# Kernel optimization log

Hardware: AMD Instinct MI355X
Metric: run time of the kernel (lower is better)

## Reference

```python
import jax, jax.numpy as jnp
import numpy as np

N, E, H, C = 50000, 1_600_000, 4, 32
DIN, DE = 128, 32
NEG_SLOPE = 0.2  # PyG GATConv leaky_relu negative_slope default


def setup_inputs() -> dict:
    key = jax.random.key(0)
    ks = jax.random.split(key, 12)
    s = 0.1  # weight scale
    return {
        "x": jax.random.normal(ks[0], (N, DIN), jnp.float32),
        "edge_index": jax.random.randint(ks[1], (2, E), 0, N, jnp.int32),
        "edge_attr": jax.random.normal(ks[2], (E, DE), jnp.float32),
        "W": jax.random.normal(ks[3], (DIN, H * C), jnp.float32) * s,
        "att_src": jax.random.normal(ks[4], (H, C), jnp.float32) * s,
        "att_dst": jax.random.normal(ks[5], (H, C), jnp.float32) * s,
        "lin_edge_W": jax.random.normal(ks[6], (DE, H * C), jnp.float32) * s,
        "att_edge": jax.random.normal(ks[7], (H, C), jnp.float32) * s,
        "bias": jax.random.normal(ks[8], (H * C,), jnp.float32) * s,
        "proj_W": jax.random.normal(ks[9], (H * C, C), jnp.float32) * s,
        "proj_b": jax.random.normal(ks[10], (C,), jnp.float32) * s,
    }


def reference(x, edge_index, edge_attr, W, att_src, att_dst, lin_edge_W,
              att_edge, bias, proj_W, proj_b):
    n = x.shape[0]
    h, c = att_src.shape
    src, dst = edge_index[0], edge_index[1]

    # add self loops; loop edge_attr = mean of incoming edge_attr (PyG fill_value='mean')
    deg = jax.ops.segment_sum(jnp.ones(src.shape, x.dtype), dst, num_segments=n)
    ea_mean = jax.ops.segment_sum(edge_attr, dst, num_segments=n) / jnp.maximum(deg, 1.0)[:, None]
    loop = jnp.arange(n, dtype=src.dtype)
    src = jnp.concatenate([src, loop])
    dst = jnp.concatenate([dst, loop])
    ea = jnp.concatenate([edge_attr, ea_mean], axis=0)

    xl = (x @ W).reshape(n, h, c)                       # [N,H,C]
    a_src = jnp.einsum('nhc,hc->nh', xl, att_src)       # [N,H]
    a_dst = jnp.einsum('nhc,hc->nh', xl, att_dst)
    e = (ea @ lin_edge_W).reshape(-1, h, c)             # [E',H,C]
    a_e = jnp.einsum('ehc,hc->eh', e, att_edge)

    alpha = jax.nn.leaky_relu(a_src[src] + a_dst[dst] + a_e, NEG_SLOPE)  # [E',H]
    amax = jax.lax.stop_gradient(jax.ops.segment_max(alpha, dst, num_segments=n))
    alpha = jnp.exp(alpha - amax[dst])
    denom = jax.ops.segment_sum(alpha, dst, num_segments=n)
    alpha = alpha / (denom[dst] + 1e-16)                # segment softmax over incoming edges

    out = jax.ops.segment_sum(xl[src] * alpha[..., None], dst, num_segments=n)  # [N,H,C]
    out = out.reshape(n, h * c) + bias                  # concat heads + bias
    return out @ proj_W + proj_b                        # concat projection
```

## Files before the change

### kernel.cpp

```cpp
#include <hip/hip_runtime.h>

#define NEG_SLOPE 0.2f

typedef float f32x4 __attribute__((ext_vector_type(4)));
typedef short bf16x8 __attribute__((ext_vector_type(8)));

__device__ __forceinline__ float lrelu(float x) { return x > 0.0f ? x : NEG_SLOPE * x; }

__device__ __forceinline__ float bcast(float v, int srcLane) {
  return __int_as_float(__builtin_amdgcn_readlane(__float_as_int(v), srcLane));
}

__device__ __forceinline__ unsigned pack_bf16(float a, float b) {
  unsigned ua = __float_as_uint(a), ub = __float_as_uint(b);
  ua += 0x7fffu + ((ua >> 16) & 1u);
  ub += 0x7fffu + ((ub >> 16) & 1u);
  return (ua >> 16) | (ub & 0xffff0000u);
}
__device__ __forceinline__ unsigned short bf16of(float a) {
  unsigned ua = __float_as_uint(a);
  ua += 0x7fffu + ((ua >> 16) & 1u);
  return (unsigned short)(ua >> 16);
}
__device__ __forceinline__ float bf16lo(unsigned z) { return __uint_as_float(z << 16); }
__device__ __forceinline__ float bf16hi(unsigned z) { return __uint_as_float(z & 0xffff0000u); }

__global__ void k0_setup(const float* __restrict__ W, const float* __restrict__ proj_W,
                         const float* __restrict__ att_src, const float* __restrict__ att_dst,
                         const float* __restrict__ lin_edge_W, const float* __restrict__ att_edge,
                         const float* __restrict__ bias, const float* __restrict__ proj_b,
                         unsigned short* __restrict__ Wzb, float* __restrict__ Ws,
                         float* __restrict__ Wd, float* __restrict__ M, float* __restrict__ cproj) {
  int t = blockIdx.x * blockDim.x + threadIdx.x;
  if (t < 16384) {
    int d = t >> 7, o = t & 127;
    int h = o >> 5, jj = o & 31;
    float s = 0.f;
    #pragma unroll
    for (int c = 0; c < 32; ++c)
      s += W[d * 128 + h * 32 + c] * proj_W[(h * 32 + c) * 32 + jj];
    Wzb[((d >> 3) * 128 + o) * 8 + (d & 7)] = bf16of(s);
  } else if (t < 16384 + 512) {
    int idx = t - 16384; int d = idx >> 2, h = idx & 3;
    float s = 0.f;
    #pragma unroll
    for (int c = 0; c < 32; ++c) s += W[d * 128 + h * 32 + c] * att_src[h * 32 + c];
    Ws[d * 4 + h] = s;
  } else if (t < 16384 + 1024) {
    int idx = t - 16384 - 512; int d = idx >> 2, h = idx & 3;
    float s = 0.f;
    #pragma unroll
    for (int c = 0; c < 32; ++c) s += W[d * 128 + h * 32 + c] * att_dst[h * 32 + c];
    Wd[d * 4 + h] = s;
  } else if (t < 16384 + 1024 + 128) {
    int idx = t - 16384 - 1024; int d = idx >> 2, h = idx & 3;
    float s = 0.f;
    #pragma unroll
    for (int c = 0; c < 32; ++c) s += lin_edge_W[d * 128 + h * 32 + c] * att_edge[h * 32 + c];
    M[d * 4 + h] = s;
  } else if (t < 16384 + 1024 + 128 + 32) {
    int jj = t - 16384 - 1024 - 128;
    float s = proj_b[jj];
    #pragma unroll
    for (int k = 0; k < 128; ++k) s += bias[k] * proj_W[k * 32 + jj];
    cproj[jj] = s;
  }
}

__global__ __launch_bounds__(256) void k3a_att(
    const float* __restrict__ x, const float* __restrict__ Ws, const float* __restrict__ Wd,
    int n, float* __restrict__ a_src, float* __restrict__ a_dst) {
  int tid = threadIdx.x;
  int lane = tid & 63, wid = tid >> 6;
  float ws0[4], ws1[4], wd0[4], wd1[4];
  #pragma unroll
  for (int h = 0; h < 4; ++h) {
    ws0[h] = Ws[lane * 4 + h];  ws1[h] = Ws[(64 + lane) * 4 + h];
    wd0[h] = Wd[lane * 4 + h];  wd1[h] = Wd[(64 + lane) * 4 + h];
  }
  int gw = blockIdx.x * 4 + wid;
  int nw = gridDim.x * 4;
  for (int base = gw * 4; base < n; base += nw * 4) {
    float xa[4], xb[4];
    #pragma unroll
    for (int u = 0; u < 4; ++u) {
      int node = base + u;
      xa[u] = (node < n) ? x[(size_t)node * 128 + lane] : 0.0f;
      xb[u] = (node < n) ? x[(size_t)node * 128 + 64 + lane] : 0.0f;
    }
    #pragma unroll
    for (int u = 0; u < 4; ++u) {
      int node = base + u;
      if (node >= n) break;
      float ps[4], pd[4];
      #pragma unroll
      for (int h = 0; h < 4; ++h) {
        ps[h] = xa[u] * ws0[h] + xb[u] * ws1[h];
        pd[h] = xa[u] * wd0[h] + xb[u] * wd1[h];
      }
      #pragma unroll
      for (int m = 1; m < 64; m <<= 1) {
        #pragma unroll
        for (int h = 0; h < 4; ++h) {
          ps[h] += __shfl_xor(ps[h], m);
          pd[h] += __shfl_xor(pd[h], m);
        }
      }
      if (lane == 0) {
        *(float4*)&a_src[node * 4] = make_float4(ps[0], ps[1], ps[2], ps[3]);
        *(float4*)&a_dst[node * 4] = make_float4(pd[0], pd[1], pd[2], pd[3]);
      }
    }
  }
}

__global__ __launch_bounds__(256) void k3b_gemm(
    const float* __restrict__ x, const unsigned short* __restrict__ Wzb,
    int n, unsigned* __restrict__ Zp) {
  __shared__ __align__(16) unsigned short WzL[16384];
  int tid = threadIdx.x;
  #pragma unroll
  for (int i = 0; i < 8; ++i)
    *(uint4*)&WzL[(i * 256 + tid) * 8] = *(const uint4*)&Wzb[(i * 256 + tid) * 8];
  __syncthreads();
  int lane = tid & 63, wid = tid >> 6;
  int rgrp = lane >> 4, rl = lane & 15;
  int r0 = blockIdx.x * 64 + wid * 16;
  if (r0 >= n) return;
  int row = r0 + rl; if (row >= n) row = n - 1;
  const float* xr = x + (size_t)row * 128 + rgrp * 8;
  bf16x8 a[4];
  #pragma unroll
  for (int q = 0; q < 4; ++q) {
    float4 v0 = *(const float4*)(xr + q * 32);
    float4 v1 = *(const float4*)(xr + q * 32 + 4);
    union { unsigned u[4]; bf16x8 v; } fa;
    fa.u[0] = pack_bf16(v0.x, v0.y); fa.u[1] = pack_bf16(v0.z, v0.w);
    fa.u[2] = pack_bf16(v1.x, v1.y); fa.u[3] = pack_bf16(v1.z, v1.w);
    a[q] = fa.v;
  }
  f32x4 acc[8];
  #pragma unroll
  for (int t = 0; t < 8; ++t) acc[t] = (f32x4){0.f, 0.f, 0.f, 0.f};
  #pragma unroll
  for (int q = 0; q < 4; ++q) {
    #pragma unroll
    for (int t = 0; t < 8; ++t) {
      bf16x8 b = *(const bf16x8*)&WzL[((q * 4 + rgrp) * 128 + t * 16 + rl) * 8];
      acc[t] = __builtin_amdgcn_mfma_f32_16x16x32_bf16(a[q], b, acc[t], 0, 0, 0);
    }
  }
  #pragma unroll
  for (int t = 0; t < 4; ++t) {
    #pragma unroll
    for (int r = 0; r < 4; ++r) {
      int rr = r0 + rgrp * 4 + r;
      if (rr < n)
        Zp[(size_t)rr * 64 + t * 16 + rl] = pack_bf16(acc[t][r], acc[t + 4][r]);
    }
  }
}

__global__ __launch_bounds__(256) void k1_edge(
    const int* __restrict__ ei, int E, const float4* __restrict__ ea4,
    const float* __restrict__ Mg,
    const float* __restrict__ a_src, const float* __restrict__ a_dst,
    uint4* __restrict__ we, int* __restrict__ deg, int* __restrict__ rank) {
  int lane = threadIdx.x & 63, wid = threadIdx.x >> 6;
  int j = lane & 7;
  const float4* Mf4 = (const float4*)Mg;
  float4 m0 = Mf4[4 * j + 0], m1 = Mf4[4 * j + 1];
  float4 m2 = Mf4[4 * j + 2], m3 = Mf4[4 * j + 3];
  int perm = 8 * (lane & 7) + (lane >> 3);
  int gw = blockIdx.x * 4 + wid, nw = gridDim.x * 4;
  int ntiles = (E + 63) >> 6;
  for (int tile = gw; tile < ntiles; tile += nw) {
    int T0 = tile << 6;
    size_t fbase = (size_t)T0 * 8;
    float cx = 0.f, cy = 0.f, cz = 0.f, cw = 0.f;
    #pragma unroll
    for (int k = 0; k < 8; ++k) {
      size_t idx = fbase + (size_t)k * 64 + lane;
      float4 v = (idx < (size_t)E * 8) ? ea4[idx] : make_float4(0.f, 0.f, 0.f, 0.f);
      float px = v.x * m0.x + v.y * m1.x + v.z * m2.x + v.w * m3.x;
      float py = v.x * m0.y + v.y * m1.y + v.z * m2.y + v.w * m3.y;
      float pz = v.x * m0.z + v.y * m1.z + v.z * m2.z + v.w * m3.z;
      float pw = v.x * m0.w + v.y * m1.w + v.z * m2.w + v.w * m3.w;
      #pragma unroll
      for (int m = 1; m < 8; m <<= 1) {
        px += __shfl_xor(px, m); py += __shfl_xor(py, m);
        pz += __shfl_xor(pz, m); pw += __shfl_xor(pw, m);
      }
      if (j == k) { cx = px; cy = py; cz = pz; cw = pw; }
    }
    int e = T0 + perm;
    if (e < E) {
      int s = ei[e], d = ei[E + e];
      int rk = atomicAdd(&deg[d], 1);
      float4 as = *(const float4*)&a_src[(size_t)s * 4];
      float4 ad = *(const float4*)&a_dst[(size_t)d * 4];
      float w0 = __expf(lrelu(cx + as.x + ad.x));
      float w1 = __expf(lrelu(cy + as.y + ad.y));
      float w2 = __expf(lrelu(cz + as.z + ad.z));
      float w3 = __expf(lrelu(cw + as.w + ad.w));
      we[e] = make_uint4(pack_bf16(w0, w1), pack_bf16(w2, w3),
                         pack_bf16(cx, cy), pack_bf16(cz, cw));
      rank[e] = rk;
    }
  }
}

__global__ __launch_bounds__(1024) void k2_scan(const int* __restrict__ deg, int n,
                                                int* __restrict__ offsets) {
  __shared__ int shw[16];
  __shared__ int shtot;
  int tid = threadIdx.x;
  int lane = tid & 63, wid = tid >> 6;
  int nch = (n + 4095) >> 12;
  int4 v[16];
  #pragma unroll
  for (int c = 0; c < 16; ++c) {
    if (c < nch) {
      int i = c * 4096 + tid * 4;
      int4 t = make_int4(0, 0, 0, 0);
      if (i + 3 < n) t = *(const int4*)&deg[i];
      else {
        if (i < n) t.x = deg[i];
        if (i + 1 < n) t.y = deg[i + 1];
        if (i + 2 < n) t.z = deg[i + 2];
        if (i + 3 < n) t.w = deg[i + 3];
      }
      v[c] = t;
    }
  }
  int running = 0;
  #pragma unroll
  for (int c = 0; c < 16; ++c) {
    if (c < nch) {
      int i = c * 4096 + tid * 4;
      int4 t = v[c];
      int tsum = t.x + t.y + t.z + t.w;
      int inc = tsum;
      #pragma unroll
      for (int s = 1; s < 64; s <<= 1) {
        int q = __shfl_up(inc, s);
        if (lane >= s) inc += q;
      }
      if (lane == 63) shw[wid] = inc;
      __syncthreads();
      if (wid == 0) {
        int w = (lane < 16) ? shw[lane] : 0;
        int winc = w;
        #pragma unroll
        for (int s = 1; s < 16; s <<= 1) {
          int q = __shfl_up(winc, s);
          if (lane >= s) winc += q;
        }
        if (lane < 16) shw[lane] = winc - w;
        if (lane == 15) shtot = winc;
      }
      __syncthreads();
      int excl = running + shw[wid] + inc - tsum;
      if (i < n)     offsets[i + 1] = excl + t.x;
      if (i + 1 < n) offsets[i + 2] = excl + t.x + t.y;
      if (i + 2 < n) offsets[i + 3] = excl + t.x + t.y + t.z;
      if (i + 3 < n) offsets[i + 4] = excl + tsum;
      running += shtot;
      __syncthreads();
    }
  }
  if (tid == 0) offsets[0] = 0;
}

__global__ void k4_scatter(const int* __restrict__ ei, int E,
                           const int* __restrict__ rank, const int* __restrict__ offsets,
                           const uint4* __restrict__ we, uint4* __restrict__ csr) {
  int e = blockIdx.x * blockDim.x + threadIdx.x;
  if (e >= E) return;
  int s = ei[e], d = ei[E + e];
  int slot = offsets[d] + rank[e];
  uint4 w = we[e];
  uint4* ent = &csr[(size_t)slot * 2];
  *(int*)ent = s;
  ent[1] = w;
}

__global__ __launch_bounds__(256) void k5_agg(
    const int* __restrict__ offsets, const uint4* __restrict__ csr,
    const unsigned* __restrict__ Zp,
    const float* __restrict__ a_src, const float* __restrict__ a_dst,
    const float* __restrict__ cproj, int n, float* __restrict__ out) {
  __shared__ float4 s_w[4][64];
  __shared__ int    s_s[4][64];
  int tid = threadIdx.x;
  int lane = tid & 63, wid = tid >> 6;
  int gw = blockIdx.x * 4 + wid, nw = gridDim.x * 4;
  int h0 = lane >> 5, j = lane & 31;
  float cp = cproj[j];
  const float* wbase = (const float*)&s_w[wid][0];
  for (int node = gw; node < n; node += nw) {
    int off0 = offsets[node], off1 = offsets[node + 1];
    int dg = off1 - off0;
    float dsx = 0.f, dsy = 0.f, dsz = 0.f, dsw = 0.f;
    float aex = 0.f, aey = 0.f, aez = 0.f, aew = 0.f;
    float agg0 = 0.f, agg1 = 0.f;
    for (int base = off0; base < off1; base += 64) {
      int rem = off1 - base; if (rem > 64) rem = 64;
      if (lane < rem) {
        const uint4* ent = &csr[(size_t)(base + lane) * 2];
        int s = *(const int*)ent;
        uint4 w = ent[1];
        float w0 = bf16lo(w.x), w1 = bf16hi(w.x);
        float w2 = bf16lo(w.y), w3 = bf16hi(w.y);
        dsx += w0; dsy += w1; dsz += w2; dsw += w3;
        aex += bf16lo(w.z); aey += bf16hi(w.z);
        aez += bf16lo(w.w); aew += bf16hi(w.w);
        s_w[wid][lane] = make_float4(w0, w2, w1, w3);
        s_s[wid][lane] = s;
      }
      int jj = 0;
      for (; jj + 4 <= rem; jj += 4) {
        int s0 = s_s[wid][jj], s1 = s_s[wid][jj + 1];
        int s2 = s_s[wid][jj + 2], s3 = s_s[wid][jj + 3];
        unsigned z0 = Zp[(size_t)s0 * 64 + lane];
        unsigned z1 = Zp[(size_t)s1 * 64 + lane];
        unsigned z2 = Zp[(size_t)s2 * 64 + lane];
        unsigned z3 = Zp[(size_t)s3 * 64 + lane];
        float2 w0 = *(const float2*)(wbase + (jj    ) * 4 + 2 * h0);
        float2 w1 = *(const float2*)(wbase + (jj + 1) * 4 + 2 * h0);
        float2 w2 = *(const float2*)(wbase + (jj + 2) * 4 + 2 * h0);
        float2 w3 = *(const float2*)(wbase + (jj + 3) * 4 + 2 * h0);
        agg0 += w0.x * bf16lo(z0) + w1.x * bf16lo(z1) + w2.x * bf16lo(z2) + w3.x * bf16lo(z3);
        agg1 += w0.y * bf16hi(z0) + w1.y * bf16hi(z1) + w2.y * bf16hi(z2) + w3.y * bf16hi(z3);
      }
      for (; jj < rem; ++jj) {
        int s0 = s_s[wid][jj];
        unsigned z0 = Zp[(size_t)s0 * 64 + lane];
        float2 w0 = *(const float2*)(wbase + jj * 4 + 2 * h0);
        agg0 += w0.x * bf16lo(z0);
        agg1 += w0.y * bf16hi(z0);
      }
    }
    #pragma unroll
    for (int m = 1; m < 64; m <<= 1) {
      dsx += __shfl_xor(dsx, m); dsy += __shfl_xor(dsy, m);
      dsz += __shfl_xor(dsz, m); dsw += __shfl_xor(dsw, m);
      aex += __shfl_xor(aex, m); aey += __shfl_xor(aey, m);
      aez += __shfl_xor(aez, m); aew += __shfl_xor(aew, m);
    }
    float invd = 1.0f / (float)(dg > 0 ? dg : 1);
    float4 asn = *(const float4*)&a_src[node * 4];
    float4 ad  = *(const float4*)&a_dst[node * 4];
    float w0 = __expf(lrelu(asn.x + ad.x + aex * invd));
    float w1 = __expf(lrelu(asn.y + ad.y + aey * invd));
    float w2 = __expf(lrelu(asn.z + ad.z + aez * invd));
    float w3 = __expf(lrelu(asn.w + ad.w + aew * invd));
    dsx += w0; dsy += w1; dsz += w2; dsw += w3;
    unsigned zpn = Zp[(size_t)node * 64 + lane];
    float sw0 = h0 ? w1 : w0, sw1 = h0 ? w3 : w2;
    agg0 += sw0 * bf16lo(zpn);
    agg1 += sw1 * bf16hi(zpn);
    float d0 = h0 ? dsy : dsx, d1 = h0 ? dsw : dsz;
    float tt = agg0 / (d0 + 1e-16f) + agg1 / (d1 + 1e-16f);
    tt += __shfl_xor(tt, 32);
    if (lane < 32) out[node * 32 + j] = tt + cp;
  }
}

extern "C" void kernel_launch(void* const* d_in, const int* in_sizes, int n_in,
                              void* d_out, int out_size, void* d_ws, size_t ws_size,
                              hipStream_t stream) {
  const float* x          = (const float*)d_in[0];
  const int*   ei         = (const int*)  d_in[1];
  const float* ea         = (const float*)d_in[2];
  const float* W          = (const float*)d_in[3];
  const float* att_src    = (const float*)d_in[4];
  const float* att_dst    = (const float*)d_in[5];
  const float* lin_edge_W = (const float*)d_in[6];
  const float* att_edge   = (const float*)d_in[7];
  const float* bias       = (const float*)d_in[8];
  const float* proj_W     = (const float*)d_in[9];
  const float* proj_b     = (const float*)d_in[10];
  float* out = (float*)d_out;
  int N = in_sizes[0] / 128;
  int E = in_sizes[1] / 2;

  char* p = (char*)d_ws;
  auto alloc = [&](size_t bytes) {
    char* r = p;
    p += (bytes + 255) & ~(size_t)255;
    return r;
  };
  unsigned* Zp          = (unsigned*)alloc((size_t)N * 64 * 4);
  float* a_src          = (float*)alloc((size_t)N * 4 * 4);
  float* a_dst          = (float*)alloc((size_t)N * 4 * 4);
  int*   deg            = (int*)  alloc((size_t)N * 4);
  int*   offsets        = (int*)  alloc((size_t)(N + 1) * 4);
  int*   rank           = (int*)  alloc((size_t)E * 4);
  uint4* we             = (uint4*)alloc((size_t)E * 16);
  uint4* csr            = (uint4*)alloc((size_t)E * 32);
  unsigned short* Wzb   = (unsigned short*)alloc(16384 * 2);
  float* Ws             = (float*)alloc(128 * 4 * 4);
  float* Wd             = (float*)alloc(128 * 4 * 4);
  float* M              = (float*)alloc(32 * 4 * 4);
  float* cproj          = (float*)alloc(32 * 4);

  hipMemsetAsync(deg, 0, (size_t)N * 4, stream);

  k0_setup<<<69, 256, 0, stream>>>(W, proj_W, att_src, att_dst, lin_edge_W, att_edge,
                                   bias, proj_b, Wzb, Ws, Wd, M, cproj);
  k3a_att<<<512, 256, 0, stream>>>(x, Ws, Wd, N, a_src, a_dst);
  k3b_gemm<<<(N + 63) / 64, 256, 0, stream>>>(x, Wzb, N, Zp);
  k1_edge<<<2048, 256, 0, stream>>>(ei, E, (const float4*)ea, M,
                                    a_src, a_dst, we, deg, rank);
  k2_scan<<<1, 1024, 0, stream>>>(deg, N, offsets);
  k4_scatter<<<(E + 255) / 256, 256, 0, stream>>>(ei, E, rank, offsets, we, csr);
  k5_agg<<<2048, 256, 0, stream>>>(offsets, csr, Zp, a_src, a_dst, cproj, N, out);
}
```

Baseline: 531.5 us.

## Split edge kernel into edge-attr projection and per-edge softmax/degree pass

Splits the fused edge kernel in two. The first kernel streams edge_attr, computes the per-edge attention logits, packs them to bf16 and stores them to a new buffer with a lane shuffle so the writes are coalesced. The second kernel is one thread per edge and does the gathers, the degree atomic, exp and rank writes. The intent is to separate the bandwidth-bound streaming from the latency-bound gather/atomic phase and improve occupancy, at the cost of an extra E*8-byte write and read plus one more launch.

```diff
diff --git a/kernel.cpp b/kernel.cpp
--- a/kernel.cpp
+++ b/kernel.cpp
@@ -6,10 +6,6 @@
 typedef short bf16x8 __attribute__((ext_vector_type(8)));
 
 __device__ __forceinline__ float lrelu(float x) { return x > 0.0f ? x : NEG_SLOPE * x; }
-
-__device__ __forceinline__ float bcast(float v, int srcLane) {
-  return __int_as_float(__builtin_amdgcn_readlane(__float_as_int(v), srcLane));
-}
 
 __device__ __forceinline__ unsigned pack_bf16(float a, float b) {
   unsigned ua = __float_as_uint(a), ub = __float_as_uint(b);
@@ -161,11 +157,9 @@
   }
 }
 
-__global__ __launch_bounds__(256) void k1_edge(
-    const int* __restrict__ ei, int E, const float4* __restrict__ ea4,
-    const float* __restrict__ Mg,
-    const float* __restrict__ a_src, const float* __restrict__ a_dst,
-    uint4* __restrict__ we, int* __restrict__ deg, int* __restrict__ rank) {
+__global__ __launch_bounds__(256) void k1a_ae(
+    const float4* __restrict__ ea4, const float* __restrict__ Mg, int E,
+    uint2* __restrict__ ae8) {
   int lane = threadIdx.x & 63, wid = threadIdx.x >> 6;
   int j = lane & 7;
   const float4* Mf4 = (const float4*)Mg;
@@ -193,21 +187,33 @@
       }
       if (j == k) { cx = px; cy = py; cz = pz; cw = pw; }
     }
-    int e = T0 + perm;
-    if (e < E) {
-      int s = ei[e], d = ei[E + e];
-      int rk = atomicAdd(&deg[d], 1);
-      float4 as = *(const float4*)&a_src[(size_t)s * 4];
-      float4 ad = *(const float4*)&a_dst[(size_t)d * 4];
-      float w0 = __expf(lrelu(cx + as.x + ad.x));
-      float w1 = __expf(lrelu(cy + as.y + ad.y));
-      float w2 = __expf(lrelu(cz + as.z + ad.z));
-      float w3 = __expf(lrelu(cw + as.w + ad.w));
-      we[e] = make_uint4(pack_bf16(w0, w1), pack_bf16(w2, w3),
-                         pack_bf16(cx, cy), pack_bf16(cz, cw));
-      rank[e] = rk;
-    }
-  }
+    unsigned p01 = pack_bf16(cx, cy), p23 = pack_bf16(cz, cw);
+    p01 = (unsigned)__shfl((int)p01, perm, 64);
+    p23 = (unsigned)__shfl((int)p23, perm, 64);
+    int e = T0 + lane;
+    if (e < E) ae8[e] = make_uint2(p01, p23);
+  }
+}
+
+__global__ __launch_bounds__(256) void k1b_edge(
+    const int* __restrict__ ei, int E, const uint2* __restrict__ ae8,
+    const float* __restrict__ a_src, const float* __restrict__ a_dst,
+    uint4* __restrict__ we, int* __restrict__ deg, int* __restrict__ rank) {
+  int e = blockIdx.x * 256 + threadIdx.x;
+  if (e >= E) return;
+  int s = ei[e], d = ei[E + e];
+  uint2 ae = ae8[e];
+  float4 as = *(const float4*)&a_src[(size_t)s * 4];
+  float4 ad = *(const float4*)&a_dst[(size_t)d * 4];
+  int rk = atomicAdd(&deg[d], 1);
+  float ae0 = bf16lo(ae.x), ae1 = bf16hi(ae.x);
+  float ae2 = bf16lo(ae.y), ae3 = bf16hi(ae.y);
+  float w0 = __expf(lrelu(ae0 + as.x + ad.x));
+  float w1 = __expf(lrelu(ae1 + as.y + ad.y));
+  float w2 = __expf(lrelu(ae2 + as.z + ad.z));
+  float w3 = __expf(lrelu(ae3 + as.w + ad.w));
+  we[e] = make_uint4(pack_bf16(w0, w1), pack_bf16(w2, w3), ae.x, ae.y);
+  rank[e] = rk;
 }
 
 __global__ __launch_bounds__(1024) void k2_scan(const int* __restrict__ deg, int n,
@@ -397,6 +403,7 @@
   int*   deg            = (int*)  alloc((size_t)N * 4);
   int*   offsets        = (int*)  alloc((size_t)(N + 1) * 4);
   int*   rank           = (int*)  alloc((size_t)E * 4);
+  uint2* ae8            = (uint2*)alloc((size_t)E * 8);
   uint4* we             = (uint4*)alloc((size_t)E * 16);
   uint4* csr            = (uint4*)alloc((size_t)E * 32);
   unsigned short* Wzb   = (unsigned short*)alloc(16384 * 2);
@@ -409,10 +416,10 @@
 
   k0_setup<<<69, 256, 0, stream>>>(W, proj_W, att_src, att_dst, lin_edge_W, att_edge,
                                    bias, proj_b, Wzb, Ws, Wd, M, cproj);
+  k1a_ae<<<2048, 256, 0, stream>>>((const float4*)ea, M, E, ae8);
   k3a_att<<<512, 256, 0, stream>>>(x, Ws, Wd, N, a_src, a_dst);
   k3b_gemm<<<(N + 63) / 64, 256, 0, stream>>>(x, Wzb, N, Zp);
-  k1_edge<<<2048, 256, 0, stream>>>(ei, E, (const float4*)ea, M,
-                                    a_src, a_dst, we, deg, rank);
+  k1b_edge<<<(E + 255) / 256, 256, 0, stream>>>(ei, E, ae8, a_src, a_dst, we, deg, rank);
   k2_scan<<<1, 1024, 0, stream>>>(deg, N, offsets);
   k4_scatter<<<(E + 255) / 256, 256, 0, stream>>>(ei, E, rank, offsets, we, csr);
   k5_agg<<<2048, 256, 0, stream>>>(offsets, csr, Zp, a_src, a_dst, cproj, N, out);
```

Measured after the change: 556.8 us. +4.8%, slower.

## Fuse attention-score projection into GEMM, hoist edge loads, widen aggregation unroll

Applied to the files above, without the earlier changes.

Removes the separate attention-logit kernel and computes a_src/a_dst inside the bf16 MFMA GEMM from the fp32 x values it already loads, so x is read once instead of twice and one launch is dropped. The edge kernel now issues the edge_attr, index, atomic and a_src/a_dst loads up front before the reduction, to overlap memory latency. The aggregation inner loop is unrolled from 4 to 8 gathered neighbours to raise memory-level parallelism. The cost is higher register pressure in all three kernels.

```diff
diff --git a/kernel.cpp b/kernel.cpp
--- a/kernel.cpp
+++ b/kernel.cpp
@@ -6,10 +6,6 @@
 typedef short bf16x8 __attribute__((ext_vector_type(8)));
 
 __device__ __forceinline__ float lrelu(float x) { return x > 0.0f ? x : NEG_SLOPE * x; }
-
-__device__ __forceinline__ float bcast(float v, int srcLane) {
-  return __int_as_float(__builtin_amdgcn_readlane(__float_as_int(v), srcLane));
-}
 
 __device__ __forceinline__ unsigned pack_bf16(float a, float b) {
   unsigned ua = __float_as_uint(a), ub = __float_as_uint(b);
@@ -67,77 +63,62 @@
   }
 }
 
-__global__ __launch_bounds__(256) void k3a_att(
-    const float* __restrict__ x, const float* __restrict__ Ws, const float* __restrict__ Wd,
-    int n, float* __restrict__ a_src, float* __restrict__ a_dst) {
-  int tid = threadIdx.x;
-  int lane = tid & 63, wid = tid >> 6;
-  float ws0[4], ws1[4], wd0[4], wd1[4];
-  #pragma unroll
-  for (int h = 0; h < 4; ++h) {
-    ws0[h] = Ws[lane * 4 + h];  ws1[h] = Ws[(64 + lane) * 4 + h];
-    wd0[h] = Wd[lane * 4 + h];  wd1[h] = Wd[(64 + lane) * 4 + h];
-  }
-  int gw = blockIdx.x * 4 + wid;
-  int nw = gridDim.x * 4;
-  for (int base = gw * 4; base < n; base += nw * 4) {
-    float xa[4], xb[4];
-    #pragma unroll
-    for (int u = 0; u < 4; ++u) {
-      int node = base + u;
-      xa[u] = (node < n) ? x[(size_t)node * 128 + lane] : 0.0f;
-      xb[u] = (node < n) ? x[(size_t)node * 128 + 64 + lane] : 0.0f;
-    }
-    #pragma unroll
-    for (int u = 0; u < 4; ++u) {
-      int node = base + u;
-      if (node >= n) break;
-      float ps[4], pd[4];
-      #pragma unroll
-      for (int h = 0; h < 4; ++h) {
-        ps[h] = xa[u] * ws0[h] + xb[u] * ws1[h];
-        pd[h] = xa[u] * wd0[h] + xb[u] * wd1[h];
-      }
-      #pragma unroll
-      for (int m = 1; m < 64; m <<= 1) {
-        #pragma unroll
-        for (int h = 0; h < 4; ++h) {
-          ps[h] += __shfl_xor(ps[h], m);
-          pd[h] += __shfl_xor(pd[h], m);
-        }
-      }
-      if (lane == 0) {
-        *(float4*)&a_src[node * 4] = make_float4(ps[0], ps[1], ps[2], ps[3]);
-        *(float4*)&a_dst[node * 4] = make_float4(pd[0], pd[1], pd[2], pd[3]);
-      }
-    }
-  }
-}
-
-__global__ __launch_bounds__(256) void k3b_gemm(
+__global__ __launch_bounds__(256) void k3_gemm(
     const float* __restrict__ x, const unsigned short* __restrict__ Wzb,
-    int n, unsigned* __restrict__ Zp) {
+    const float* __restrict__ Ws, const float* __restrict__ Wd,
+    int n, unsigned* __restrict__ Zp, float* __restrict__ a_src, float* __restrict__ a_dst) {
   __shared__ __align__(16) unsigned short WzL[16384];
+  __shared__ float4 WsL[128];
+  __shared__ float4 WdL[128];
   int tid = threadIdx.x;
   #pragma unroll
   for (int i = 0; i < 8; ++i)
     *(uint4*)&WzL[(i * 256 + tid) * 8] = *(const uint4*)&Wzb[(i * 256 + tid) * 8];
+  if (tid < 128) {
+    WsL[tid] = ((const float4*)Ws)[tid];
+    WdL[tid] = ((const float4*)Wd)[tid];
+  }
   __syncthreads();
   int lane = tid & 63, wid = tid >> 6;
   int rgrp = lane >> 4, rl = lane & 15;
   int r0 = blockIdx.x * 64 + wid * 16;
   if (r0 >= n) return;
-  int row = r0 + rl; if (row >= n) row = n - 1;
-  const float* xr = x + (size_t)row * 128 + rgrp * 8;
+  int row = r0 + rl;
+  bool rowok = row < n;
+  int rowc = rowok ? row : n - 1;
+  const float* xr = x + (size_t)rowc * 128 + rgrp * 8;
   bf16x8 a[4];
+  float ps[4] = {0.f, 0.f, 0.f, 0.f}, pd[4] = {0.f, 0.f, 0.f, 0.f};
   #pragma unroll
   for (int q = 0; q < 4; ++q) {
     float4 v0 = *(const float4*)(xr + q * 32);
     float4 v1 = *(const float4*)(xr + q * 32 + 4);
+    int d0 = q * 32 + rgrp * 8;
+    float vv[8] = {v0.x, v0.y, v0.z, v0.w, v1.x, v1.y, v1.z, v1.w};
+    #pragma unroll
+    for (int i = 0; i < 8; ++i) {
+      float4 ws = WsL[d0 + i], wd = WdL[d0 + i];
+      ps[0] += vv[i] * ws.x; ps[1] += vv[i] * ws.y;
+      ps[2] += vv[i] * ws.z; ps[3] += vv[i] * ws.w;
+      pd[0] += vv[i] * wd.x; pd[1] += vv[i] * wd.y;
+      pd[2] += vv[i] * wd.z; pd[3] += vv[i] * wd.w;
+    }
     union { unsigned u[4]; bf16x8 v; } fa;
     fa.u[0] = pack_bf16(v0.x, v0.y); fa.u[1] = pack_bf16(v0.z, v0.w);
     fa.u[2] = pack_bf16(v1.x, v1.y); fa.u[3] = pack_bf16(v1.z, v1.w);
     a[q] = fa.v;
+  }
+  #pragma unroll
+  for (int m = 16; m < 64; m <<= 1) {
+    #pragma unroll
+    for (int h = 0; h < 4; ++h) {
+      ps[h] += __shfl_xor(ps[h], m);
+      pd[h] += __shfl_xor(pd[h], m);
+    }
+  }
+  if (rgrp == 0 && rowok) {
+    *(float4*)&a_src[(size_t)row * 4] = make_float4(ps[0], ps[1], ps[2], ps[3]);
+    *(float4*)&a_dst[(size_t)row * 4] = make_float4(pd[0], pd[1], pd[2], pd[3]);
   }
   f32x4 acc[8];
   #pragma unroll
@@ -176,16 +157,37 @@
   int ntiles = (E + 63) >> 6;
   for (int tile = gw; tile < ntiles; tile += nw) {
     int T0 = tile << 6;
+    int e = T0 + perm;
     size_t fbase = (size_t)T0 * 8;
+    int s = 0, d = 0;
+    bool ok = e < E;
+    if (ok) { s = ei[e]; d = ei[E + e]; }
+    float4 v[8];
+    if (T0 + 64 <= E) {
+      #pragma unroll
+      for (int k = 0; k < 8; ++k) v[k] = ea4[fbase + (size_t)k * 64 + lane];
+    } else {
+      #pragma unroll
+      for (int k = 0; k < 8; ++k) {
+        size_t idx = fbase + (size_t)k * 64 + lane;
+        v[k] = (idx < (size_t)E * 8) ? ea4[idx] : make_float4(0.f, 0.f, 0.f, 0.f);
+      }
+    }
+    int rk = 0;
+    float4 as = make_float4(0.f, 0.f, 0.f, 0.f);
+    float4 ad = make_float4(0.f, 0.f, 0.f, 0.f);
+    if (ok) {
+      rk = atomicAdd(&deg[d], 1);
+      as = *(const float4*)&a_src[(size_t)s * 4];
+      ad = *(const float4*)&a_dst[(size_t)d * 4];
+    }
     float cx = 0.f, cy = 0.f, cz = 0.f, cw = 0.f;
     #pragma unroll
     for (int k = 0; k < 8; ++k) {
-      size_t idx = fbase + (size_t)k * 64 + lane;
-      float4 v = (idx < (size_t)E * 8) ? ea4[idx] : make_float4(0.f, 0.f, 0.f, 0.f);
-      float px = v.x * m0.x + v.y * m1.x + v.z * m2.x + v.w * m3.x;
-      float py = v.x * m0.y + v.y * m1.y + v.z * m2.y + v.w * m3.y;
-      float pz = v.x * m0.z + v.y * m1.z + v.z * m2.z + v.w * m3.z;
-      float pw = v.x * m0.w + v.y * m1.w + v.z * m2.w + v.w * m3.w;
+      float px = v[k].x * m0.x + v[k].y * m1.x + v[k].z * m2.x + v[k].w * m3.x;
+      float py = v[k].x * m0.y + v[k].y * m1.y + v[k].z * m2.y + v[k].w * m3.y;
+      float pz = v[k].x * m0.z + v[k].y * m1.z + v[k].z * m2.z + v[k].w * m3.z;
+      float pw = v[k].x * m0.w + v[k].y * m1.w + v[k].z * m2.w + v[k].w * m3.w;
       #pragma unroll
       for (int m = 1; m < 8; m <<= 1) {
         px += __shfl_xor(px, m); py += __shfl_xor(py, m);
@@ -193,12 +195,7 @@
       }
       if (j == k) { cx = px; cy = py; cz = pz; cw = pw; }
     }
-    int e = T0 + perm;
-    if (e < E) {
-      int s = ei[e], d = ei[E + e];
-      int rk = atomicAdd(&deg[d], 1);
-      float4 as = *(const float4*)&a_src[(size_t)s * 4];
-      float4 ad = *(const float4*)&a_dst[(size_t)d * 4];
+    if (ok) {
       float w0 = __expf(lrelu(cx + as.x + ad.x));
       float w1 = __expf(lrelu(cy + as.y + ad.y));
       float w2 = __expf(lrelu(cz + as.z + ad.z));
@@ -319,19 +316,19 @@
         s_s[wid][lane] = s;
       }
       int jj = 0;
-      for (; jj + 4 <= rem; jj += 4) {
-        int s0 = s_s[wid][jj], s1 = s_s[wid][jj + 1];
-        int s2 = s_s[wid][jj + 2], s3 = s_s[wid][jj + 3];
-        unsigned z0 = Zp[(size_t)s0 * 64 + lane];
-        unsigned z1 = Zp[(size_t)s1 * 64 + lane];
-        unsigned z2 = Zp[(size_t)s2 * 64 + lane];
-        unsigned z3 = Zp[(size_t)s3 * 64 + lane];
-        float2 w0 = *(const float2*)(wbase + (jj    ) * 4 + 2 * h0);
-        float2 w1 = *(const float2*)(wbase + (jj + 1) * 4 + 2 * h0);
-        float2 w2 = *(const float2*)(wbase + (jj + 2) * 4 + 2 * h0);
-        float2 w3 = *(const float2*)(wbase + (jj + 3) * 4 + 2 * h0);
-        agg0 += w0.x * bf16lo(z0) + w1.x * bf16lo(z1) + w2.x * bf16lo(z2) + w3.x * bf16lo(z3);
-        agg1 += w0.y * bf16hi(z0) + w1.y * bf16hi(z1) + w2.y * bf16hi(z2) + w3.y * bf16hi(z3);
+      for (; jj + 8 <= rem; jj += 8) {
+        int ss[8];
+        #pragma unroll
+        for (int u = 0; u < 8; ++u) ss[u] = s_s[wid][jj + u];
+        unsigned z[8];
+        #pragma unroll
+        for (int u = 0; u < 8; ++u) z[u] = Zp[(size_t)ss[u] * 64 + lane];
+        #pragma unroll
+        for (int u = 0; u < 8; ++u) {
+          float2 w = *(const float2*)(wbase + (jj + u) * 4 + 2 * h0);
+          agg0 += w.x * bf16lo(z[u]);
+          agg1 += w.y * bf16hi(z[u]);
+        }
       }
       for (; jj < rem; ++jj) {
         int s0 = s_s[wid][jj];
@@ -409,8 +406,7 @@
 
   k0_setup<<<69, 256, 0, stream>>>(W, proj_W, att_src, att_dst, lin_edge_W, att_edge,
                                    bias, proj_b, Wzb, Ws, Wd, M, cproj);
-  k3a_att<<<512, 256, 0, stream>>>(x, Ws, Wd, N, a_src, a_dst);
-  k3b_gemm<<<(N + 63) / 64, 256, 0, stream>>>(x, Wzb, N, Zp);
+  k3_gemm<<<(N + 63) / 64, 256, 0, stream>>>(x, Wzb, Ws, Wd, N, Zp, a_src, a_dst);
   k1_edge<<<2048, 256, 0, stream>>>(ei, E, (const float4*)ea, M,
                                     a_src, a_dst, we, deg, rank);
   k2_scan<<<1, 1024, 0, stream>>>(deg, N, offsets);
```

Measured after the change: 487.1 us. 1.09x faster.
